# Optimization experiments

Hardware: AMD Instinct MI355X
Metric: run time of the kernel (lower is better)

Reference implementation:

```python
import jax, jax.numpy as jnp
import numpy as np

N = 8192
NFEAT = 512
NHID = 256
NCLASS = 40
EDGE_P = 0.002  # ~16 avg degree


def setup_inputs() -> dict:
    key = jax.random.key(0)
    k1, k2, k3, k4 = jax.random.split(key, 4)
    x = jax.random.normal(k1, (N, NFEAT), dtype=jnp.float32)
    # unnormalized binary adjacency without self loops (module adds eye itself)
    adj = (jax.random.uniform(k2, (N, N)) < EDGE_P).astype(jnp.float32)
    # GCNConv weights: torch.rand(in, out) -> uniform[0,1)
    W1 = jax.random.uniform(k3, (NFEAT, NHID), dtype=jnp.float32)
    W2 = jax.random.uniform(k4, (NHID, NCLASS), dtype=jnp.float32)
    return {"x": x, "adj": adj, "W1": W1, "W2": W2}


def reference(x, adj, W1, W2):
    n = adj.shape[0]
    # add self loops: in_adj.to_dense() + eye
    A_hat = adj + jnp.eye(n, dtype=adj.dtype)
    # normalize_adj: D^{-1/2} A_hat D^{-1/2} (diag matmuls == row/col scaling)
    d = A_hat.sum(-1) ** -0.5  # [N]
    norm_adj = d[:, None] * A_hat * d[None, :]
    # conv1: relu(adj @ x @ W1); dropout is identity in eval mode
    h = jax.nn.relu((norm_adj @ x) @ W1)
    # conv2 reuses the same normalized adjacency (only one DGG layer by default)
    h2 = jax.nn.relu((norm_adj @ h) @ W2)
    return jax.nn.log_softmax(h2, axis=-1)
```

## Files before the change

### kernel.cpp

```cpp
#include <hip/hip_runtime.h>
#include <math.h>

#define NV 8192
#define CAP 64

__global__ __launch_bounds__(256) void build_graph(
    const float* __restrict__ adj, int* __restrict__ cols,
    int* __restrict__ rowcount, float* __restrict__ dinv,
    float* __restrict__ diagv) {
  int row = blockIdx.x;
  int t = threadIdx.x;
  int lane = t & 63;
  __shared__ int cnt;
  __shared__ int diag_nz;
  __shared__ int wsum[4];
  if (t == 0) { cnt = 0; diag_nz = 0; }
  __syncthreads();
  const float4* arow = (const float4*)(adj + (size_t)row * NV);
  int mycount = 0;
  for (int i = t; i < NV / 4; i += 256) {
    float4 v = arow[i];
    float va[4] = {v.x, v.y, v.z, v.w};
#pragma unroll
    for (int j = 0; j < 4; j++) {
      bool nz = (va[j] != 0.0f);
      mycount += nz ? 1 : 0;
      int c = i * 4 + j;
      bool isdiag = nz && (c == row);
      bool take = nz && !isdiag;
      if (isdiag) diag_nz = 1;
      unsigned long long m = __ballot(take);
      if (m != 0ull) {
        int tot = __popcll(m);
        int pre = __popcll(m & ((1ull << lane) - 1ull));
        int leader = __ffsll((unsigned long long)m) - 1;
        int base = 0;
        if (lane == leader) base = atomicAdd(&cnt, tot);
        base = __shfl(base, leader, 64);
        if (take) {
          int p = base + pre;
          if (p < CAP) cols[(size_t)row * CAP + p] = c;
        }
      }
    }
  }
  for (int off = 32; off > 0; off >>= 1) mycount += __shfl_xor(mycount, off, 64);
  if (lane == 0) wsum[t >> 6] = mycount;
  __syncthreads();
  if (t == 0) {
    int nnz = wsum[0] + wsum[1] + wsum[2] + wsum[3];
    float deg = (float)nnz + 1.0f;
    dinv[row] = 1.0f / sqrtf(deg);
    diagv[row] = diag_nz ? 2.0f : 1.0f;
    rowcount[row] = cnt > CAP ? CAP : cnt;
  }
}

__global__ __launch_bounds__(256) void gemm_f32(
    const float* __restrict__ A, const float* __restrict__ B,
    float* __restrict__ C, int M, int K, int Nvalid, int ldb, int ldc) {
  __shared__ float As[16][68];
  __shared__ float Bs[16][64];
  int t = threadIdx.x;
  int bm0 = blockIdx.y * 64;
  int bn0 = blockIdx.x * 64;
  int tx = t & 15, ty = t >> 4;
  int ar = t >> 2;
  int ak = (t & 3) * 4;
  int bk = t >> 4;
  int bn = (t & 15) * 4;
  float acc[4][4] = {};
  for (int k0 = 0; k0 < K; k0 += 16) {
    float4 av = *(const float4*)(A + (size_t)(bm0 + ar) * K + k0 + ak);
    float4 bv;
    int bc = bn0 + bn;
    if (bc + 3 < Nvalid) {
      bv = *(const float4*)(B + (size_t)(k0 + bk) * ldb + bc);
    } else {
      bv.x = (bc + 0 < Nvalid) ? B[(size_t)(k0 + bk) * ldb + bc + 0] : 0.0f;
      bv.y = (bc + 1 < Nvalid) ? B[(size_t)(k0 + bk) * ldb + bc + 1] : 0.0f;
      bv.z = (bc + 2 < Nvalid) ? B[(size_t)(k0 + bk) * ldb + bc + 2] : 0.0f;
      bv.w = (bc + 3 < Nvalid) ? B[(size_t)(k0 + bk) * ldb + bc + 3] : 0.0f;
    }
    As[ak + 0][ar] = av.x;
    As[ak + 1][ar] = av.y;
    As[ak + 2][ar] = av.z;
    As[ak + 3][ar] = av.w;
    *(float4*)(&Bs[bk][bn]) = bv;
    __syncthreads();
#pragma unroll
    for (int kk = 0; kk < 16; kk++) {
      float4 a = *(const float4*)(&As[kk][ty * 4]);
      float4 b = *(const float4*)(&Bs[kk][tx * 4]);
      acc[0][0] += a.x * b.x; acc[0][1] += a.x * b.y; acc[0][2] += a.x * b.z; acc[0][3] += a.x * b.w;
      acc[1][0] += a.y * b.x; acc[1][1] += a.y * b.y; acc[1][2] += a.y * b.z; acc[1][3] += a.y * b.w;
      acc[2][0] += a.z * b.x; acc[2][1] += a.z * b.y; acc[2][2] += a.z * b.z; acc[2][3] += a.z * b.w;
      acc[3][0] += a.w * b.x; acc[3][1] += a.w * b.y; acc[3][2] += a.w * b.z; acc[3][3] += a.w * b.w;
    }
    __syncthreads();
  }
#pragma unroll
  for (int i = 0; i < 4; i++) {
    *(float4*)(C + (size_t)(bm0 + ty * 4 + i) * ldc + bn0 + tx * 4) =
        make_float4(acc[i][0], acc[i][1], acc[i][2], acc[i][3]);
  }
}

__global__ __launch_bounds__(256) void spmm_relu_k(
    const float* __restrict__ Z, const int* __restrict__ cols,
    const int* __restrict__ rowcount, const float* __restrict__ dinv,
    const float* __restrict__ diagv, float* __restrict__ H) {
  int lane = threadIdx.x & 63;
  int row = blockIdx.x * 4 + (threadIdx.x >> 6);
  const float4* Zr = (const float4*)Z;
  float di = dinv[row];
  float4 z = Zr[(size_t)row * 64 + lane];
  float dd = diagv[row] * di;
  float4 acc;
  acc.x = dd * z.x; acc.y = dd * z.y; acc.z = dd * z.z; acc.w = dd * z.w;
  int cnt = rowcount[row];
  const int* cr = cols + (size_t)row * CAP;
  int e = 0;
  for (; e + 4 <= cnt; e += 4) {
    int c0 = cr[e + 0], c1 = cr[e + 1], c2 = cr[e + 2], c3 = cr[e + 3];
    float w0 = dinv[c0], w1 = dinv[c1], w2 = dinv[c2], w3 = dinv[c3];
    float4 g0 = Zr[(size_t)c0 * 64 + lane];
    float4 g1 = Zr[(size_t)c1 * 64 + lane];
    float4 g2 = Zr[(size_t)c2 * 64 + lane];
    float4 g3 = Zr[(size_t)c3 * 64 + lane];
    acc.x += w0 * g0.x + w1 * g1.x + w2 * g2.x + w3 * g3.x;
    acc.y += w0 * g0.y + w1 * g1.y + w2 * g2.y + w3 * g3.y;
    acc.z += w0 * g0.z + w1 * g1.z + w2 * g2.z + w3 * g3.z;
    acc.w += w0 * g0.w + w1 * g1.w + w2 * g2.w + w3 * g3.w;
  }
  for (; e < cnt; e++) {
    int c = cr[e];
    float w = dinv[c];
    float4 g = Zr[(size_t)c * 64 + lane];
    acc.x += w * g.x; acc.y += w * g.y; acc.z += w * g.z; acc.w += w * g.w;
  }
  float4 o;
  o.x = fmaxf(acc.x * di, 0.0f);
  o.y = fmaxf(acc.y * di, 0.0f);
  o.z = fmaxf(acc.z * di, 0.0f);
  o.w = fmaxf(acc.w * di, 0.0f);
  ((float4*)H)[(size_t)row * 64 + lane] = o;
}

__global__ __launch_bounds__(256) void spmm2_lsm_k(
    const float* __restrict__ Z, const int* __restrict__ cols,
    const int* __restrict__ rowcount, const float* __restrict__ dinv,
    const float* __restrict__ diagv, float* __restrict__ out) {
  int lane = threadIdx.x & 63;
  int row = blockIdx.x * 4 + (threadIdx.x >> 6);
  float di = dinv[row];
  float acc = diagv[row] * di * Z[(size_t)row * 64 + lane];
  int cnt = rowcount[row];
  const int* cr = cols + (size_t)row * CAP;
  int e = 0;
  for (; e + 4 <= cnt; e += 4) {
    int c0 = cr[e + 0], c1 = cr[e + 1], c2 = cr[e + 2], c3 = cr[e + 3];
    float w0 = dinv[c0], w1 = dinv[c1], w2 = dinv[c2], w3 = dinv[c3];
    float g0 = Z[(size_t)c0 * 64 + lane];
    float g1 = Z[(size_t)c1 * 64 + lane];
    float g2 = Z[(size_t)c2 * 64 + lane];
    float g3 = Z[(size_t)c3 * 64 + lane];
    acc += w0 * g0 + w1 * g1 + w2 * g2 + w3 * g3;
  }
  for (; e < cnt; e++) {
    int c = cr[e];
    acc += dinv[c] * Z[(size_t)c * 64 + lane];
  }
  float h2 = (lane < 40) ? fmaxf(acc * di, 0.0f) : -INFINITY;
  float m = h2;
  for (int off = 32; off > 0; off >>= 1) m = fmaxf(m, __shfl_xor(m, off, 64));
  float ex = (lane < 40) ? expf(h2 - m) : 0.0f;
  float s = ex;
  for (int off = 32; off > 0; off >>= 1) s += __shfl_xor(s, off, 64);
  float ls = logf(s);
  if (lane < 40) out[(size_t)row * 40 + lane] = h2 - m - ls;
}

extern "C" void kernel_launch(void* const* d_in, const int* in_sizes, int n_in,
                              void* d_out, int out_size, void* d_ws, size_t ws_size,
                              hipStream_t stream) {
  (void)in_sizes; (void)n_in; (void)out_size; (void)ws_size;
  const float* x   = (const float*)d_in[0];
  const float* adj = (const float*)d_in[1];
  const float* W1  = (const float*)d_in[2];
  const float* W2  = (const float*)d_in[3];
  float* out = (float*)d_out;
  char* ws = (char*)d_ws;

  int*   cols     = (int*)(ws);
  int*   rowcount = (int*)(ws + 2097152);
  float* dinv     = (float*)(ws + 2129920);
  float* diagv    = (float*)(ws + 2162688);
  float* XW1      = (float*)(ws + 2195456);
  float* H        = (float*)(ws + 10584064);
  float* HW2      = (float*)(ws + 18972672);

  hipLaunchKernelGGL(build_graph, dim3(NV), dim3(256), 0, stream,
                     adj, cols, rowcount, dinv, diagv);
  hipLaunchKernelGGL(gemm_f32, dim3(4, 128), dim3(256), 0, stream,
                     x, W1, XW1, NV, 512, 256, 256, 256);
  hipLaunchKernelGGL(spmm_relu_k, dim3(NV / 4), dim3(256), 0, stream,
                     XW1, cols, rowcount, dinv, diagv, H);
  hipLaunchKernelGGL(gemm_f32, dim3(1, 128), dim3(256), 0, stream,
                     H, W2, HW2, NV, 256, 40, 40, 64);
  hipLaunchKernelGGL(spmm2_lsm_k, dim3(NV / 4), dim3(256), 0, stream,
                     HW2, cols, rowcount, dinv, diagv, out);
}
```

Measured before the change: 451.4 us.

## Run X@W1 on bf16 MFMA using a three-term split-precision product

Replaces the fp32 SIMT GEMM for x@W1 with a matrix-core GEMM. Inputs are first split into bf16 high and low parts by two new conversion kernels, with W1 stored transposed. The GEMM then accumulates hi*hi + lo*hi + hi*lo to approximate fp32 accuracy. This adds two extra launches and extra memory traffic for the split copies in exchange for faster matrix-core math. The spmm2 gather expression is also rewritten inline, with no change in behaviour.

```diff
diff --git a/kernel.cpp b/kernel.cpp
--- a/kernel.cpp
+++ b/kernel.cpp
@@ -3,6 +3,18 @@
 
 #define NV 8192
 #define CAP 64
+
+typedef __attribute__((ext_vector_type(8))) short short8;
+typedef __attribute__((ext_vector_type(4))) float f32x4;
+
+static __device__ __forceinline__ unsigned short f2bf(float v) {
+  unsigned int u = __float_as_uint(v);
+  unsigned int r = (u + 0x7fffu + ((u >> 16) & 1u)) >> 16;
+  return (unsigned short)r;
+}
+static __device__ __forceinline__ float bf2f(unsigned short h) {
+  return __uint_as_float(((unsigned int)h) << 16);
+}
 
 __global__ __launch_bounds__(256) void build_graph(
     const float* __restrict__ adj, int* __restrict__ cols,
@@ -54,6 +66,91 @@
     diagv[row] = diag_nz ? 2.0f : 1.0f;
     rowcount[row] = cnt > CAP ? CAP : cnt;
   }
+}
+
+__global__ __launch_bounds__(256) void split_a(
+    const float* __restrict__ x, unsigned short* __restrict__ Ah,
+    unsigned short* __restrict__ Al) {
+  int i = blockIdx.x * 256 + threadIdx.x;
+  float4 v = ((const float4*)x)[i];
+  ushort4 h, l;
+  h.x = f2bf(v.x); l.x = f2bf(v.x - bf2f(h.x));
+  h.y = f2bf(v.y); l.y = f2bf(v.y - bf2f(h.y));
+  h.z = f2bf(v.z); l.z = f2bf(v.z - bf2f(h.z));
+  h.w = f2bf(v.w); l.w = f2bf(v.w - bf2f(h.w));
+  ((ushort4*)Ah)[i] = h;
+  ((ushort4*)Al)[i] = l;
+}
+
+__global__ __launch_bounds__(256) void split_w1t(
+    const float* __restrict__ W1, unsigned short* __restrict__ Bh,
+    unsigned short* __restrict__ Bl) {
+  int n = blockIdx.x;
+  int k = blockIdx.y * 256 + threadIdx.x;
+  float v = W1[(size_t)k * 256 + n];
+  unsigned short h = f2bf(v);
+  Bh[(size_t)n * 512 + k] = h;
+  Bl[(size_t)n * 512 + k] = f2bf(v - bf2f(h));
+}
+
+__global__ __launch_bounds__(256) void gemm1_mfma(
+    const unsigned short* __restrict__ Ah, const unsigned short* __restrict__ Al,
+    const unsigned short* __restrict__ Bh, const unsigned short* __restrict__ Bl,
+    float* __restrict__ C) {
+  const int K = 512;
+  __shared__ __align__(16) unsigned short sAh[128][40];
+  __shared__ __align__(16) unsigned short sAl[128][40];
+  __shared__ __align__(16) unsigned short sBh[64][40];
+  __shared__ __align__(16) unsigned short sBl[64][40];
+  int t = threadIdx.x;
+  int bn = blockIdx.x * 64;
+  int bm = blockIdx.y * 128;
+  int lane = t & 63, w = t >> 6;
+  int quad = lane >> 4, m16 = lane & 15;
+  f32x4 acc[2][4] = {};
+  for (int k0 = 0; k0 < K; k0 += 32) {
+#pragma unroll
+    for (int i = 0; i < 2; i++) {
+      int id = t + i * 256;
+      int row = id >> 2, q = id & 3;
+      *(uint4*)&sAh[row][q * 8] = *(const uint4*)&Ah[(size_t)(bm + row) * K + k0 + q * 8];
+      *(uint4*)&sAl[row][q * 8] = *(const uint4*)&Al[(size_t)(bm + row) * K + k0 + q * 8];
+    }
+    {
+      int row = t >> 2, q = t & 3;
+      *(uint4*)&sBh[row][q * 8] = *(const uint4*)&Bh[(size_t)(bn + row) * K + k0 + q * 8];
+      *(uint4*)&sBl[row][q * 8] = *(const uint4*)&Bl[(size_t)(bn + row) * K + k0 + q * 8];
+    }
+    __syncthreads();
+    short8 ah[2], al[2], bh[4], bl[4];
+#pragma unroll
+    for (int i = 0; i < 2; i++) {
+      ah[i] = *(const short8*)&sAh[w * 32 + i * 16 + m16][quad * 8];
+      al[i] = *(const short8*)&sAl[w * 32 + i * 16 + m16][quad * 8];
+    }
+#pragma unroll
+    for (int j = 0; j < 4; j++) {
+      bh[j] = *(const short8*)&sBh[j * 16 + m16][quad * 8];
+      bl[j] = *(const short8*)&sBl[j * 16 + m16][quad * 8];
+    }
+#pragma unroll
+    for (int i = 0; i < 2; i++)
+#pragma unroll
+      for (int j = 0; j < 4; j++) {
+        acc[i][j] = __builtin_amdgcn_mfma_f32_16x16x32_bf16(ah[i], bh[j], acc[i][j], 0, 0, 0);
+        acc[i][j] = __builtin_amdgcn_mfma_f32_16x16x32_bf16(al[i], bh[j], acc[i][j], 0, 0, 0);
+        acc[i][j] = __builtin_amdgcn_mfma_f32_16x16x32_bf16(ah[i], bl[j], acc[i][j], 0, 0, 0);
+      }
+    __syncthreads();
+  }
+#pragma unroll
+  for (int i = 0; i < 2; i++)
+#pragma unroll
+    for (int j = 0; j < 4; j++)
+#pragma unroll
+      for (int r = 0; r < 4; r++)
+        C[(size_t)(bm + w * 32 + i * 16 + quad * 4 + r) * 256 + bn + j * 16 + m16] =
+            acc[i][j][r];
 }
 
 __global__ __launch_bounds__(256) void gemm_f32(
@@ -161,11 +258,8 @@
   for (; e + 4 <= cnt; e += 4) {
     int c0 = cr[e + 0], c1 = cr[e + 1], c2 = cr[e + 2], c3 = cr[e + 3];
     float w0 = dinv[c0], w1 = dinv[c1], w2 = dinv[c2], w3 = dinv[c3];
-    float g0 = Z[(size_t)c0 * 64 + lane];
-    float g1 = Z[(size_t)c1 * 64 + lane];
-    float g2 = Z[(size_t)c2 * 64 + lane];
-    float g3 = Z[(size_t)c3 * 64 + lane];
-    acc += w0 * g0 + w1 * g1 + w2 * g2 + w3 * g3;
+    acc += w0 * Z[(size_t)c0 * 64 + lane] + w1 * Z[(size_t)c1 * 64 + lane] +
+           w2 * Z[(size_t)c2 * 64 + lane] + w3 * Z[(size_t)c3 * 64 + lane];
   }
   for (; e < cnt; e++) {
     int c = cr[e];
@@ -199,11 +293,19 @@
   float* XW1      = (float*)(ws + 2195456);
   float* H        = (float*)(ws + 10584064);
   float* HW2      = (float*)(ws + 18972672);
+  unsigned short* Ah = (unsigned short*)(ws + 21069824);
+  unsigned short* Al = (unsigned short*)(ws + 29458432);
+  unsigned short* Bh = (unsigned short*)(ws + 37847040);
+  unsigned short* Bl = (unsigned short*)(ws + 38109184);
 
   hipLaunchKernelGGL(build_graph, dim3(NV), dim3(256), 0, stream,
                      adj, cols, rowcount, dinv, diagv);
-  hipLaunchKernelGGL(gemm_f32, dim3(4, 128), dim3(256), 0, stream,
-                     x, W1, XW1, NV, 512, 256, 256, 256);
+  hipLaunchKernelGGL(split_a, dim3(NV * 512 / 4 / 256), dim3(256), 0, stream,
+                     x, Ah, Al);
+  hipLaunchKernelGGL(split_w1t, dim3(256, 2), dim3(256), 0, stream,
+                     W1, Bh, Bl);
+  hipLaunchKernelGGL(gemm1_mfma, dim3(4, 64), dim3(256), 0, stream,
+                     Ah, Al, Bh, Bl, XW1);
   hipLaunchKernelGGL(spmm_relu_k, dim3(NV / 4), dim3(256), 0, stream,
                      XW1, cols, rowcount, dinv, diagv, H);
   hipLaunchKernelGGL(gemm_f32, dim3(1, 128), dim3(256), 0, stream,
```

After: 437.9 us. 1.03x faster.
